# Performance work log

Measured on AMD Instinct MI355X. Metric: run time of the kernel, lower is better.

The kernel has to match this reference:

```python
import jax, jax.numpy as jnp
import numpy as np

N = 50000
E = 1600000
IN_C, HID, OUT_C = 128, 128, 64
NUM_HIDDEN = 3  # extra hidden GCN layers after the first


def setup_inputs() -> dict:
    key = jax.random.key(0)
    ks = jax.random.split(key, 16)
    inp = {}
    inp["x"] = jax.random.normal(ks[0], (N, IN_C), dtype=jnp.float32)
    inp["edge_index"] = jax.random.randint(ks[1], (2, E), 0, N, dtype=jnp.int64)
    # GCN stack weights (glorot-ish scale)
    def w(k, fi, fo):
        return jax.random.normal(k, (fi, fo), dtype=jnp.float32) * (1.0 / np.sqrt(fi))
    inp["W0"] = w(ks[2], IN_C, HID); inp["b0"] = jnp.zeros((HID,), jnp.float32)
    inp["W1"] = w(ks[3], HID, HID);  inp["b1"] = jnp.zeros((HID,), jnp.float32)
    inp["W2"] = w(ks[4], HID, HID);  inp["b2"] = jnp.zeros((HID,), jnp.float32)
    inp["W3"] = w(ks[5], HID, HID);  inp["b3"] = jnp.zeros((HID,), jnp.float32)
    inp["Wmu"] = w(ks[6], HID, OUT_C); inp["bmu"] = jnp.zeros((OUT_C,), jnp.float32)
    inp["Wlv"] = w(ks[7], HID, OUT_C); inp["blv"] = jnp.zeros((OUT_C,), jnp.float32)
    return inp


def _gcn_norm(edge_index, n):
    # PyG gcn_norm: add self-loops, deg over targets, sym normalization.
    loops = jnp.arange(n, dtype=edge_index.dtype)
    src = jnp.concatenate([edge_index[0], loops])
    dst = jnp.concatenate([edge_index[1], loops])
    deg = jax.ops.segment_sum(jnp.ones_like(src, dtype=jnp.float32), dst, num_segments=n)
    dis = jnp.where(deg > 0, jax.lax.rsqrt(jnp.maximum(deg, 1.0)), 0.0)
    norm = dis[src] * dis[dst]  # [E+N]
    return src, dst, norm


def _gcn_conv(x, W, b, src, dst, norm, n):
    h = x @ W                      # [N, out]
    msg = h[src] * norm[:, None]   # gather + scale, [E+N, out]
    return jax.ops.segment_sum(msg, dst, num_segments=n) + b


def reference(x, edge_index, W0, b0, W1, b1, W2, b2, W3, b3, Wmu, bmu, Wlv, blv):
    n = x.shape[0]
    src, dst, norm = _gcn_norm(edge_index, n)
    # layer 0: selu
    h = jax.nn.selu(_gcn_conv(x, W0, b0, src, dst, norm, n))
    # middle layers: silu (default act)
    h = jax.nn.silu(_gcn_conv(h, W1, b1, src, dst, norm, n))
    h = jax.nn.silu(_gcn_conv(h, W2, b2, src, dst, norm, n))
    # last gc layer: log(sigmoid(.))
    h = jax.nn.log_sigmoid(_gcn_conv(h, W3, b3, src, dst, norm, n))
    mu_z = _gcn_conv(h, Wmu, bmu, src, dst, norm, n)
    logvar_z = _gcn_conv(h, Wlv, blv, src, dst, norm, n)
    return (mu_z, logvar_z)
```

## Files before the change

kernel.cpp:

```cpp
#include <hip/hip_runtime.h>
#include <hip/hip_bf16.h>
#include <hip/hip_fp8.h>
#include <cstddef>

#define HIDC 128
#define ELL 80
#define ELL_S 96
#define XB_S 136
#define WT_S 136
#define CST8 144

typedef __attribute__((ext_vector_type(8))) short bf16x8;
typedef __attribute__((ext_vector_type(4))) float f32x4;
typedef __attribute__((ext_vector_type(2))) float f32x2;

static __device__ inline unsigned short f2bf(float f) {
    __hip_bfloat16 b = __float2bfloat16(f);
    return *(unsigned short*)&b;
}
static __device__ inline unsigned char f2fp8(float f) {
    __hip_fp8_e4m3 q(f);
    return (unsigned char)q.__x;
}
static __device__ inline float fp82f(unsigned char b) {
    __hip_fp8_e4m3 q;
    q.__x = (__hip_fp8_storage_t)b;
    return (float)q;
}

__global__ void probe_fmt_kernel(const void* ei, int E, int N, int* flag) {
    __shared__ int bad;
    if (threadIdx.x == 0) bad = 0;
    __syncthreads();
    const long long* p = (const long long*)ei;
    int limit = E < 1024 ? E : 1024;
    for (int i = threadIdx.x; i < limit; i += blockDim.x) {
        long long v = p[i];
        if (v < 0 || v >= (long long)N) atomicOr(&bad, 1);
    }
    __syncthreads();
    if (threadIdx.x == 0) flag[0] = (bad ? 0 : 1);
}

__global__ void zero_kernel(int* a, int n) {
    int i = blockIdx.x * blockDim.x + threadIdx.x;
    if (i < n) a[i] = 0;
}

__global__ __launch_bounds__(256) void pack_kernel(
    const int* __restrict__ ei32, const int* __restrict__ lo64,
    const int* __restrict__ flag, unsigned short* __restrict__ src16,
    unsigned short* __restrict__ dst16, int E) {
    int i2 = (blockIdx.x * 256 + threadIdx.x) * 2;
    if (i2 >= E) return;
    int is64 = flag[0];
    unsigned int s0, s1, d0, d1;
    if (i2 + 1 < E) {
        if (is64) {
            uint4 sv = *(const uint4*)(lo64 + 2 * (size_t)i2);
            uint4 dv = *(const uint4*)(lo64 + 2 * ((size_t)E + i2));
            s0 = sv.x; s1 = sv.z; d0 = dv.x; d1 = dv.z;
        } else {
            uint2 sv = *(const uint2*)(ei32 + (size_t)i2);
            uint2 dv = *(const uint2*)(ei32 + (size_t)E + i2);
            s0 = sv.x; s1 = sv.y; d0 = dv.x; d1 = dv.y;
        }
        *(unsigned int*)(src16 + i2) = (s0 & 0xffffu) | (s1 << 16);
        *(unsigned int*)(dst16 + i2) = (d0 & 0xffffu) | (d1 << 16);
    } else {
        if (is64) {
            s0 = (unsigned int)lo64[2 * (size_t)i2];
            d0 = (unsigned int)lo64[2 * ((size_t)E + i2)];
        } else {
            s0 = (unsigned int)ei32[i2];
            d0 = (unsigned int)ei32[(size_t)E + i2];
        }
        src16[i2] = (unsigned short)s0;
        dst16[i2] = (unsigned short)d0;
    }
}

__global__ __launch_bounds__(256) void scatter_part_kernel(
    const unsigned short* __restrict__ src16, const unsigned short* __restrict__ dst16,
    int* cnt, unsigned short* __restrict__ ell, int E, int nchunk,
    unsigned int magic) {
    unsigned int part = blockIdx.x & 7;
    int chunk = blockIdx.x >> 3;
    int per = ((E + nchunk - 1) / nchunk + 1) & ~1;
    int e0 = chunk * per;
    int e1 = e0 + per;
    if (e1 > E) e1 = E;
    const unsigned int* dp = (const unsigned int*)dst16;
    for (int i = e0 + (int)threadIdx.x * 2; i < e1; i += 512) {
        unsigned int dd = dp[i >> 1];
        unsigned int d0 = dd & 0xffffu, d1 = dd >> 16;
        if (__umulhi(d0, magic) == part) {
            int s = src16[i];
            int k = atomicAdd(&cnt[d0], 1);
            if (k < ELL) ell[(size_t)d0 * ELL_S + k] = (unsigned short)s;
        }
        if (i + 1 < e1 && __umulhi(d1, magic) == part) {
            int s = src16[i + 1];
            int k = atomicAdd(&cnt[d1], 1);
            if (k < ELL) ell[(size_t)d1 * ELL_S + k] = (unsigned short)s;
        }
    }
}

__global__ void dis_pad_kernel(const int* __restrict__ cnt, float* __restrict__ dis,
                               unsigned short* __restrict__ ell,
                               unsigned char* __restrict__ Ht8z,
                               unsigned char* __restrict__ Ht8bz, int N) {
    int i = blockIdx.x * blockDim.x + threadIdx.x;
    if (i < N) {
        int c = cnt[i];
        dis[i] = rsqrtf((float)(c + 1));
        int cc = c < ELL ? c : ELL;
        unsigned short* row = ell + (size_t)i * ELL_S;
        row[cc] = (unsigned short)i;
        int p8 = (cc + 1 + 7) & ~7;
        for (int k = cc + 1; k < p8; ++k) row[k] = (unsigned short)N;
    }
    if (blockIdx.x == 0) {
        int t = threadIdx.x;
        if (t < 32) ((unsigned int*)(Ht8z + (size_t)N * HIDC))[t] = 0u;
        else if (t < 64) ((unsigned int*)(Ht8bz + (size_t)N * HIDC))[t - 32] = 0u;
    }
}

template <int F32IN, int FINALW, int FP8OUT, int F32OUT>
__global__ __launch_bounds__(256) void gemm_mfma(
    const void* Xv, const float* __restrict__ Wa, const float* __restrict__ Wb,
    const float* __restrict__ dis, void* __restrict__ HtV, int N,
    const float* __restrict__ bia, const float* __restrict__ bib) {
    __shared__ __align__(16) unsigned short Xb[64 * XB_S];
    __shared__ __align__(16) unsigned short Wt[128 * WT_S];
    int t = threadIdx.x;
    int row0 = blockIdx.x * 64;

    {
        int k = t >> 1, c0 = (t & 1) * 64;
        const float* src = FINALW ? ((c0 == 0) ? (Wa + (size_t)k * 64)
                                               : (Wb + (size_t)k * 64))
                                  : (Wa + (size_t)k * HIDC + c0);
#pragma unroll
        for (int i = 0; i < 64; i += 4) {
            float4 v = *(const float4*)(src + i);
            Wt[(c0 + i + 0) * WT_S + k] = f2bf(v.x);
            Wt[(c0 + i + 1) * WT_S + k] = f2bf(v.y);
            Wt[(c0 + i + 2) * WT_S + k] = f2bf(v.z);
            Wt[(c0 + i + 3) * WT_S + k] = f2bf(v.w);
        }
    }
    {
        int idx = t * 32;
        int r = idx >> 7, c = idx & 127;
        int g = row0 + r; if (g >= N) g = N - 1;
        if (F32IN) {
            const float* xs = (const float*)Xv + (size_t)g * HIDC + c;
#pragma unroll
            for (int i = 0; i < 32; i += 4) {
                float4 v = *(const float4*)(xs + i);
                Xb[r * XB_S + c + i + 0] = f2bf(v.x);
                Xb[r * XB_S + c + i + 1] = f2bf(v.y);
                Xb[r * XB_S + c + i + 2] = f2bf(v.z);
                Xb[r * XB_S + c + i + 3] = f2bf(v.w);
            }
        } else {
            const unsigned short* xs = (const unsigned short*)Xv + (size_t)g * HIDC + c;
#pragma unroll
            for (int i = 0; i < 32; i += 8) {
                ushort4 a = *(const ushort4*)(xs + i);
                ushort4 b = *(const ushort4*)(xs + i + 4);
                *(ushort4*)(Xb + r * XB_S + c + i) = a;
                *(ushort4*)(Xb + r * XB_S + c + i + 4) = b;
            }
        }
    }
    __syncthreads();

    int w = t >> 6, l = t & 63;
    int lr = l & 15, lk = l >> 4;
    f32x4 acc[8];
#pragma unroll
    for (int c = 0; c < 8; ++c) acc[c] = (f32x4){0.f, 0.f, 0.f, 0.f};

    const unsigned short* xrow = Xb + (w * 16 + lr) * XB_S + lk * 8;
    const unsigned short* wcol = Wt + lr * WT_S + lk * 8;
#pragma unroll
    for (int ks = 0; ks < 4; ++ks) {
        bf16x8 a = *(const bf16x8*)(xrow + ks * 32);
#pragma unroll
        for (int c = 0; c < 8; ++c) {
            bf16x8 b = *(const bf16x8*)(wcol + (size_t)c * 16 * WT_S + ks * 32);
            acc[c] = __builtin_amdgcn_mfma_f32_16x16x32_bf16(a, b, acc[c], 0, 0, 0);
        }
    }
    __syncthreads();

    if (F32OUT) {
        float bb[8];
#pragma unroll
        for (int c = 0; c < 8; ++c) {
            int col = c * 16 + lr;
            bb[c] = (col < 64) ? bia[col] : bib[col - 64];
        }
        float* stg = (float*)((char*)Wt + (size_t)w * 32 * WT_S * 2);
#pragma unroll
        for (int c = 0; c < 8; ++c)
#pragma unroll
            for (int r = 0; r < 4; ++r)
                stg[(lk * 4 + r) * 132 + c * 16 + lr] = acc[c][r] + bb[c];
        __syncthreads();
        int r2 = l >> 5, hh = (l >> 4) & 1, li = l & 15;
        float* muO = (float*)HtV;
        float* lvO = muO + (size_t)N * 64;
#pragma unroll
        for (int p = 0; p < 8; ++p) {
            int lrow = p * 2 + r2;
            int grow = row0 + w * 16 + lrow;
            if (grow < N) {
                const float* sp = stg + lrow * 132 + hh * 64 + li * 4;
                float4 v = *(const float4*)sp;
                float* dst = (hh ? lvO : muO) + (size_t)grow * 64 + li * 4;
                *(float4*)dst = v;
            }
        }
        return;
    }

    float dd[4];
    int rbase = row0 + w * 16 + lk * 4;
#pragma unroll
    for (int r = 0; r < 4; ++r) {
        int g = rbase + r; if (g >= N) g = N - 1;
        dd[r] = dis[g];
    }
    if (FP8OUT) {
        char* cstB = (char*)Xb + (size_t)(w * 16) * CST8;
#pragma unroll
        for (int c = 0; c < 8; ++c)
#pragma unroll
            for (int r = 0; r < 4; ++r)
                cstB[(lk * 4 + r) * CST8 + c * 16 + lr] =
                    (char)f2fp8(acc[c][r] * dd[r]);
        __syncthreads();
        int sr = l >> 2, cc = (l & 3) * 32;
        int grow = row0 + w * 16 + sr;
        if (grow < N) {
            unsigned char* dst = (unsigned char*)HtV + (size_t)grow * HIDC + cc;
            const char* srcp = (const char*)Xb + (size_t)(w * 16 + sr) * CST8 + cc;
            *(uint4*)dst = *(const uint4*)srcp;
            *(uint4*)(dst + 16) = *(const uint4*)(srcp + 16);
        }
    } else {
        unsigned short* cst = Xb + (size_t)(w * 16) * XB_S;
#pragma unroll
        for (int c = 0; c < 8; ++c)
#pragma unroll
            for (int r = 0; r < 4; ++r)
                cst[(lk * 4 + r) * XB_S + c * 16 + lr] = f2bf(acc[c][r] * dd[r]);
        __syncthreads();
        int sr = l >> 2, cc = (l & 3) * 32;
        int grow = row0 + w * 16 + sr;
        if (grow < N) {
            unsigned short* dst = (unsigned short*)HtV + (size_t)grow * HIDC + cc;
            const unsigned short* srcp = cst + sr * XB_S + cc;
#pragma unroll
            for (int u = 0; u < 32; u += 8)
                *(uint4*)(dst + u) = *(const uint4*)(srcp + u);
        }
    }
}

template <int ACT> __device__ inline float act_fn(float v) {
    if (ACT == 0)
        return 1.0507009873554805f * (v > 0.0f ? v : 1.6732632423543772f * expm1f(v));
    else if (ACT == 1)
        return v / (1.0f + expf(-v));
    else if (ACT == 2)
        return v < 0.0f ? v - log1pf(expf(v)) : -log1pf(expf(-v));
    return v;
}

template <int ACT, int OMODE>
__global__ __launch_bounds__(256) void agg_fp8(
    const unsigned char* __restrict__ Ht8, const unsigned short* __restrict__ ell,
    const int* __restrict__ cnt, const float* __restrict__ dis,
    const float* __restrict__ ba, void* __restrict__ Out, int N) {
    __shared__ __align__(16) unsigned short lrowA[4][ELL_S];
    int wv = threadIdx.x >> 6;
    int wid = blockIdx.x * 4 + wv;
    if (wid >= N) wid = N - 1;
    int lane = threadIdx.x & 63;
    unsigned int lo2 = (unsigned int)(lane * 2);

    unsigned short* lr = lrowA[wv];
    {
        const unsigned int* rs = (const unsigned int*)(ell + (size_t)wid * ELL_S);
        if (lane < ELL_S / 2) ((unsigned int*)lr)[lane] = rs[lane];
    }

    int deg = cnt[wid];
    int tot = (deg < ELL ? deg : ELL) + 1;
    int p8 = (tot + 7) & ~7;

    f32x2 ac[4];
#pragma unroll
    for (int i = 0; i < 4; ++i) ac[i] = (f32x2){0.f, 0.f};

    for (int e = 0; e < p8; e += 8) {
        uint4 w4 = *(const uint4*)(lr + e);
        unsigned int ss[8] = {w4.x & 0xffffu, w4.x >> 16, w4.y & 0xffffu, w4.y >> 16,
                              w4.z & 0xffffu, w4.z >> 16, w4.w & 0xffffu, w4.w >> 16};
#pragma unroll
        for (int j = 0; j < 8; ++j) {
            unsigned int off = (ss[j] << 7) + lo2;
            unsigned int v = *(const unsigned short*)(Ht8 + off);
#if __has_builtin(__builtin_amdgcn_cvt_pk_f32_fp8)
            ac[j & 3] += __builtin_amdgcn_cvt_pk_f32_fp8(v, false);
#else
            ac[j & 3].x += fp82f(v & 0xff);
            ac[j & 3].y += fp82f((v >> 8) & 0xff);
#endif
        }
    }

    f32x2 A = (ac[0] + ac[1]) + (ac[2] + ac[3]);
    float dd = dis[wid];

    if (OMODE == 2) {
        unsigned int o = (unsigned int)f2bf(dd * A.x) |
                         ((unsigned int)f2bf(dd * A.y) << 16);
        *(unsigned int*)((unsigned short*)Out + (size_t)wid * HIDC + lane * 2) = o;
    } else {
        float2 b2 = *(const float2*)(ba + lane * 2);
        float h0 = act_fn<ACT>(dd * A.x + b2.x);
        float h1 = act_fn<ACT>(dd * A.y + b2.y);
        if (OMODE == 0) {
            unsigned int o = (unsigned int)f2bf(h0) | ((unsigned int)f2bf(h1) << 16);
            *(unsigned int*)((unsigned short*)Out + (size_t)wid * HIDC + lane * 2) = o;
        } else {
            unsigned short o = (unsigned short)f2fp8(dd * h0) |
                               ((unsigned short)f2fp8(dd * h1) << 8);
            *(unsigned short*)((unsigned char*)Out + (size_t)wid * HIDC + lane * 2) = o;
        }
    }
}

extern "C" void kernel_launch(void* const* d_in, const int* in_sizes, int n_in,
                              void* d_out, int out_size, void* d_ws, size_t ws_size,
                              hipStream_t stream) {
    const float* x   = (const float*)d_in[0];
    const void*  ei  = d_in[1];
    const float* W0  = (const float*)d_in[2];
    const float* b0  = (const float*)d_in[3];
    const float* W1  = (const float*)d_in[4];
    const float* b1  = (const float*)d_in[5];
    const float* W2  = (const float*)d_in[6];
    const float* b2  = (const float*)d_in[7];
    const float* W3  = (const float*)d_in[8];
    const float* b3  = (const float*)d_in[9];
    const float* Wmu = (const float*)d_in[10];
    const float* bmu = (const float*)d_in[11];
    const float* Wlv = (const float*)d_in[12];
    const float* blv = (const float*)d_in[13];
    int N = in_sizes[0] / HIDC;
    int E = in_sizes[1] / 2;

    char* w = (char*)d_ws;
    size_t o = 0;
    auto alloc = [&](size_t bytes) {
        void* p = w + o;
        o = (o + bytes + 255) & ~(size_t)255;
        return p;
    };
    int*   flag = (int*)alloc(4);
    int*   cnt  = (int*)alloc((size_t)N * 4);
    unsigned short* ell = (unsigned short*)alloc((size_t)N * ELL_S * 2);
    float* dis  = (float*)alloc((size_t)N * 4);
    unsigned char* Ht8  = (unsigned char*)alloc((size_t)(N + 1) * HIDC);
    unsigned char* Ht8b = (unsigned char*)alloc((size_t)(N + 1) * HIDC);
    unsigned short* bufA = (unsigned short*)alloc((size_t)N * HIDC * 2);
    unsigned short* src16 = (unsigned short*)alloc((size_t)E * 2);
    unsigned short* dst16 = (unsigned short*)alloc((size_t)E * 2);
    (void)ws_size; (void)n_in; (void)out_size;

    const int* ei32 = (const int*)ei;
    const int* lo64 = (const int*)ei;

    int gN = (N + 255) / 256;
    int gGemm = (N + 63) / 64;
    int gAgg = (N + 3) / 4;
    int gPack = (E / 2 + 255) / 256;

    unsigned int magic = (unsigned int)(((8ULL << 32) + N - 1) / (unsigned long long)N);
    int nchunk = 256;

    probe_fmt_kernel<<<1, 256, 0, stream>>>(ei, E, N, flag);
    zero_kernel<<<gN, 256, 0, stream>>>(cnt, N);
    pack_kernel<<<gPack, 256, 0, stream>>>(ei32, lo64, flag, src16, dst16, E);
    scatter_part_kernel<<<nchunk * 8, 256, 0, stream>>>(src16, dst16, cnt, ell,
                                                        E, nchunk, magic);
    dis_pad_kernel<<<gN, 256, 0, stream>>>(cnt, dis, ell, Ht8, Ht8b, N);

    gemm_mfma<1, 0, 1, 0><<<gGemm, 256, 0, stream>>>(x, W0, nullptr, dis, Ht8, N,
                                                     nullptr, nullptr);
    agg_fp8<0, 0><<<gAgg, 256, 0, stream>>>(Ht8, ell, cnt, dis, b0, bufA, N);
    gemm_mfma<0, 0, 1, 0><<<gGemm, 256, 0, stream>>>(bufA, W1, nullptr, dis, Ht8, N,
                                                     nullptr, nullptr);
    agg_fp8<1, 0><<<gAgg, 256, 0, stream>>>(Ht8, ell, cnt, dis, b1, bufA, N);
    gemm_mfma<0, 0, 1, 0><<<gGemm, 256, 0, stream>>>(bufA, W2, nullptr, dis, Ht8, N,
                                                     nullptr, nullptr);
    agg_fp8<1, 0><<<gAgg, 256, 0, stream>>>(Ht8, ell, cnt, dis, b2, bufA, N);
    gemm_mfma<0, 0, 1, 0><<<gGemm, 256, 0, stream>>>(bufA, W3, nullptr, dis, Ht8, N,
                                                     nullptr, nullptr);
    agg_fp8<2, 1><<<gAgg, 256, 0, stream>>>(Ht8, ell, cnt, dis, b3, Ht8b, N);
    agg_fp8<3, 2><<<gAgg, 256, 0, stream>>>(Ht8b, ell, cnt, dis, nullptr, bufA, N);
    gemm_mfma<0, 1, 0, 1><<<gGemm, 256, 0, stream>>>(bufA, Wmu, Wlv, dis,
                                                     (float*)d_out, N, bmu, blv);
}
```

Before: 333.7 us.

## Build ELL adjacency with per-block node ranges and LDS counters

Replaces the partitioned global-atomic scatter with a kernel where each of 256 blocks owns a contiguous node range and scans all edges, counting in-range edges with shared-memory atomics before writing counts to global memory once. This drops the separate zero kernel and the global atomic traffic on cnt. In exchange every block reads the full dst array (256 full passes over E, largely L2-served), and npb must stay at or below 256, which holds only for N up to 65536.

```diff
diff --git a/kernel.cpp b/kernel.cpp
--- a/kernel.cpp
+++ b/kernel.cpp
@@ -9,6 +9,7 @@
 #define XB_S 136
 #define WT_S 136
 #define CST8 144
+#define NB_SC 256
 
 typedef __attribute__((ext_vector_type(8))) short bf16x8;
 typedef __attribute__((ext_vector_type(4))) float f32x4;
@@ -40,11 +41,6 @@
     }
     __syncthreads();
     if (threadIdx.x == 0) flag[0] = (bad ? 0 : 1);
-}
-
-__global__ void zero_kernel(int* a, int n) {
-    int i = blockIdx.x * blockDim.x + threadIdx.x;
-    if (i < n) a[i] = 0;
 }
 
 __global__ __launch_bounds__(256) void pack_kernel(
@@ -80,31 +76,43 @@
     }
 }
 
-__global__ __launch_bounds__(256) void scatter_part_kernel(
+__global__ __launch_bounds__(256) void scatter_range_kernel(
     const unsigned short* __restrict__ src16, const unsigned short* __restrict__ dst16,
-    int* cnt, unsigned short* __restrict__ ell, int E, int nchunk,
-    unsigned int magic) {
-    unsigned int part = blockIdx.x & 7;
-    int chunk = blockIdx.x >> 3;
-    int per = ((E + nchunk - 1) / nchunk + 1) & ~1;
-    int e0 = chunk * per;
-    int e1 = e0 + per;
-    if (e1 > E) e1 = E;
-    const unsigned int* dp = (const unsigned int*)dst16;
-    for (int i = e0 + (int)threadIdx.x * 2; i < e1; i += 512) {
-        unsigned int dd = dp[i >> 1];
-        unsigned int d0 = dd & 0xffffu, d1 = dd >> 16;
-        if (__umulhi(d0, magic) == part) {
+    int* __restrict__ cnt, unsigned short* __restrict__ ell, int E, int N) {
+    __shared__ int lcnt[256];
+    int tid = threadIdx.x;
+    int npb = (N + NB_SC - 1) / NB_SC;
+    unsigned int lo = (unsigned int)(blockIdx.x * npb);
+    lcnt[tid] = 0;
+    __syncthreads();
+
+    const uint2* dp2 = (const uint2*)dst16;
+    int G = E >> 2;
+    for (int g = tid; g < G; g += 256) {
+        uint2 v = dp2[g];
+        unsigned int dd[4] = {v.x & 0xffffu, v.x >> 16, v.y & 0xffffu, v.y >> 16};
+#pragma unroll
+        for (int j = 0; j < 4; ++j) {
+            unsigned int r = dd[j] - lo;
+            if (r < (unsigned int)npb) {
+                int s = src16[g * 4 + j];
+                int k = atomicAdd(&lcnt[r], 1);
+                if (k < ELL)
+                    ell[(size_t)(lo + r) * ELL_S + k] = (unsigned short)s;
+            }
+        }
+    }
+    for (int i = (E & ~3) + tid; i < E; i += 256) {
+        unsigned int r = (unsigned int)dst16[i] - lo;
+        if (r < (unsigned int)npb) {
             int s = src16[i];
-            int k = atomicAdd(&cnt[d0], 1);
-            if (k < ELL) ell[(size_t)d0 * ELL_S + k] = (unsigned short)s;
-        }
-        if (i + 1 < e1 && __umulhi(d1, magic) == part) {
-            int s = src16[i + 1];
-            int k = atomicAdd(&cnt[d1], 1);
-            if (k < ELL) ell[(size_t)d1 * ELL_S + k] = (unsigned short)s;
-        }
-    }
+            int k = atomicAdd(&lcnt[r], 1);
+            if (k < ELL) ell[(size_t)(lo + r) * ELL_S + k] = (unsigned short)s;
+        }
+    }
+    __syncthreads();
+    int node = (int)lo + tid;
+    if (tid < npb && node < N) cnt[node] = lcnt[tid];
 }
 
 __global__ void dis_pad_kernel(const int* __restrict__ cnt, float* __restrict__ dis,
@@ -394,14 +402,9 @@
     int gAgg = (N + 3) / 4;
     int gPack = (E / 2 + 255) / 256;
 
-    unsigned int magic = (unsigned int)(((8ULL << 32) + N - 1) / (unsigned long long)N);
-    int nchunk = 256;
-
     probe_fmt_kernel<<<1, 256, 0, stream>>>(ei, E, N, flag);
-    zero_kernel<<<gN, 256, 0, stream>>>(cnt, N);
     pack_kernel<<<gPack, 256, 0, stream>>>(ei32, lo64, flag, src16, dst16, E);
-    scatter_part_kernel<<<nchunk * 8, 256, 0, stream>>>(src16, dst16, cnt, ell,
-                                                        E, nchunk, magic);
+    scatter_range_kernel<<<NB_SC, 256, 0, stream>>>(src16, dst16, cnt, ell, E, N);
     dis_pad_kernel<<<gN, 256, 0, stream>>>(cnt, dis, ell, Ht8, Ht8b, N);
 
     gemm_mfma<1, 0, 1, 0><<<gGemm, 256, 0, stream>>>(x, W0, nullptr, dis, Ht8, N,
```

Result: slower. 864.7 us (+159.1%).
